# Performance work log

Hardware: AMD Instinct MI355X
Metric: run time of the kernel (lower is better)

The kernel has to match this reference:

```python
import math
import jax, jax.numpy as jnp
import numpy as np

NH = 16          # num_attention_heads
MAX_REL = 512    # max_relative_positions


def _t4(x):
    # [B, N, H] -> [B, NH, N, H/NH]  (transpose_for_scores)
    B, N, H = x.shape
    return x.reshape(B, N, NH, -1).transpose(0, 2, 1, 3)


def setup_inputs() -> dict:
    key = jax.random.key(0)
    ks = jax.random.split(key, 6)
    B, N, H = 1, 2048, 1024
    hidden_states = jax.random.normal(ks[0], (B, N, H), jnp.float32)
    attention_mask = jnp.ones((B, 1, N, N), jnp.int32)
    ids = jnp.arange(N, dtype=jnp.int32)
    relative_pos = ids[:, None] - ids[None, :]              # [N, N], build_relative_position
    rel_embeddings = jax.random.normal(ks[1], (2 * MAX_REL, H), jnp.float32) * 0.02
    in_proj_w = jax.random.normal(ks[2], (3 * H, H), jnp.float32) * 0.02
    q_bias = jnp.zeros((H,), jnp.float32)
    v_bias = jnp.zeros((H,), jnp.float32)
    pos_proj_w = jax.random.normal(ks[3], (H, H), jnp.float32) * 0.02
    pos_q_proj_w = jax.random.normal(ks[4], (H, H), jnp.float32) * 0.02
    pos_q_proj_b = jnp.zeros((H,), jnp.float32)
    return dict(hidden_states=hidden_states, attention_mask=attention_mask,
                relative_pos=relative_pos, rel_embeddings=rel_embeddings,
                in_proj_w=in_proj_w, q_bias=q_bias, v_bias=v_bias,
                pos_proj_w=pos_proj_w, pos_q_proj_w=pos_q_proj_w,
                pos_q_proj_b=pos_q_proj_b)


def reference(hidden_states, attention_mask, relative_pos, rel_embeddings,
              in_proj_w, q_bias, v_bias, pos_proj_w, pos_q_proj_w, pos_q_proj_b):
    B, N, H = hidden_states.shape
    dh = H // NH
    scale_factor = 1 + 2  # 1 + len(["c2p", "p2c"])
    scale = math.sqrt(dh * scale_factor)

    # fused QKV projection; chunk(3, dim=-1) AFTER transpose_for_scores -> per-head q|k|v layout
    qp = hidden_states @ in_proj_w.T                          # [B, N, 3H]
    q, k, v = jnp.split(_t4(qp), 3, axis=-1)                  # each [B, NH, N, dh]
    q = q + _t4(q_bias[None, None, :])
    v = v + _t4(v_bias[None, None, :])
    q = q / scale

    scores = jnp.einsum('bhqd,bhkd->bhqk', q, k)              # content-content

    # disentangled relative-position bias
    span = min(N, MAX_REL)                                    # att_span
    rel = rel_embeddings[MAX_REL - span:MAX_REL + span][None] # [1, 2S, H]
    rpos = relative_pos.astype(jnp.int32)[None, None]         # [1, 1, N, N]

    # c2p: content-to-position
    pos_k = _t4(rel @ pos_proj_w.T)                           # [1, NH, 2S, dh]
    c2p = jnp.einsum('bhqd,xhsd->bhqs', q, pos_k)             # [B, NH, N, 2S]
    c2p_pos = jnp.clip(rpos + span, 0, 2 * span - 1)
    c2p = jnp.take_along_axis(c2p, c2p_pos, axis=-1)          # gather -> [B, NH, N, N]

    # p2c: position-to-content
    pos_q = _t4(rel @ pos_q_proj_w.T + pos_q_proj_b) / scale  # [1, NH, 2S, dh]
    p2c = jnp.einsum('bhkd,xhsd->bhks', k, pos_q)             # [B, NH, N, 2S]
    p2c_pos = jnp.clip(-rpos + span, 0, 2 * span - 1)
    p2c = jnp.take_along_axis(p2c, p2c_pos, axis=-1)          # [B, NH, K, Q]
    p2c = jnp.swapaxes(p2c, -1, -2)                           # -> [B, NH, Q, K]

    scores = scores + c2p + p2c

    # XSoftmax: masked softmax, masked probs zeroed
    m = attention_mask.astype(bool)                           # [B, 1, N, N]
    probs = jax.nn.softmax(jnp.where(m, scores, -jnp.inf), axis=-1)
    probs = jnp.where(m, probs, 0.0)

    ctx = jnp.einsum('bhqk,bhkd->bhqd', probs, v)             # [B, NH, N, dh]
    return ctx.transpose(0, 2, 1, 3).reshape(B, N, H)
```

## Files before the change

kernel.cpp:

```cpp
#include <hip/hip_runtime.h>
#include <hip/hip_bf16.h>

typedef __bf16 bf16;
typedef __attribute__((ext_vector_type(8))) __bf16 bf16x8;
typedef __attribute__((ext_vector_type(8))) float f32x8;
typedef __attribute__((ext_vector_type(4))) float f32x4;

#define MFMA(a,b,c) __builtin_amdgcn_mfma_f32_16x16x32_bf16((a),(b),(c),0,0,0)

__device__ __forceinline__ bf16x8 ld8(const bf16* p){ bf16x8 v; __builtin_memcpy(&v,p,16); return v; }
__device__ __forceinline__ void   st8(bf16* p, bf16x8 v){ __builtin_memcpy(p,&v,16); }

__global__ __launch_bounds__(256)
void cvt_kernel(const float* __restrict__ s0, const float* __restrict__ s1,
                const float* __restrict__ s2, const float* __restrict__ s3,
                const float* __restrict__ s4,
                bf16* d0, bf16* d1, bf16* d2, bf16* d3, bf16* d4)
{
    const int sizes[5] = {2097152, 3145728, 1048576, 1048576, 1048576};
    const float* s; bf16* d;
    switch (blockIdx.y) {
        case 0: s = s0; d = d0; break;  case 1: s = s1; d = d1; break;
        case 2: s = s2; d = d2; break;  case 3: s = s3; d = d3; break;
        default: s = s4; d = d4;
    }
    const int n = sizes[blockIdx.y];
    const int stride = gridDim.x * 256 * 8;
    for (int i = (blockIdx.x * 256 + threadIdx.x) * 8; i < n; i += stride) {
        f32x8 v; __builtin_memcpy(&v, s + i, 32);
        bf16x8 r;
        #pragma unroll
        for (int j = 0; j < 8; j++) r[j] = (bf16)v[j];
        st8(d + i, r);
    }
}

__global__ __launch_bounds__(256)
void gemm_stage(const bf16* __restrict__ A, const bf16* __restrict__ Bpk,
                const bf16* __restrict__ Bpq, int K, int mode,
                const float* __restrict__ qb, const float* __restrict__ vb,
                bf16* __restrict__ o0, bf16* __restrict__ o1, bf16* __restrict__ o2,
                float* __restrict__ part)
{
    __shared__ __attribute__((aligned(16))) bf16 As[128][32];
    __shared__ __attribute__((aligned(16))) bf16 Bs[128][32];

    const int tid = threadIdx.x, w = tid >> 6, lane = tid & 63;
    const int l15 = lane & 15, quad = lane >> 4;
    const int wr = w >> 1, wc = w & 1;

    int arr = 0, my = blockIdx.y, kbeg = 0, kend = K;
    const bf16* B = Bpk;
    if (mode == 1) {
        arr = my >> 3; my &= 7;
        B = arr ? Bpq : Bpk;
        kbeg = blockIdx.z * 256; kend = kbeg + 256;
    }
    const int m0 = my * 128, n0 = blockIdx.x * 128;
    const int srow = tid >> 2, scol = (tid & 3) * 8;

    f32x4 acc[4][4] = {};
    for (int k0 = kbeg; k0 < kend; k0 += 32) {
        __syncthreads();
        st8(&As[srow][scol],    ld8(A + (size_t)(m0 + srow) * K + k0 + scol));
        st8(&As[srow+64][scol], ld8(A + (size_t)(m0 + 64 + srow) * K + k0 + scol));
        st8(&Bs[srow][scol],    ld8(B + (size_t)(n0 + srow) * K + k0 + scol));
        st8(&Bs[srow+64][scol], ld8(B + (size_t)(n0 + 64 + srow) * K + k0 + scol));
        __syncthreads();
        bf16x8 a[4], b[4];
        #pragma unroll
        for (int i = 0; i < 4; i++) a[i] = ld8(&As[wr*64 + i*16 + l15][quad*8]);
        #pragma unroll
        for (int j = 0; j < 4; j++) b[j] = ld8(&Bs[wc*64 + j*16 + l15][quad*8]);
        #pragma unroll
        for (int i = 0; i < 4; i++)
            #pragma unroll
            for (int j = 0; j < 4; j++)
                acc[i][j] = MFMA(a[i], b[j], acc[i][j]);
    }

    const float inv_scale = 0.07216878364870323f;
    #pragma unroll
    for (int i = 0; i < 4; i++) {
        #pragma unroll
        for (int j = 0; j < 4; j++) {
            #pragma unroll
            for (int r = 0; r < 4; r++) {
                int row = m0 + wr*64 + i*16 + quad*4 + r;
                int col = n0 + wc*64 + j*16 + l15;
                float v = acc[i][j][r];
                if (mode == 0) {
                    int h = col / 192, rr = col % 192;
                    if (rr < 64)
                        o0[((size_t)h*2048 + row)*64 + rr] =
                            (bf16)((v + qb[h*64 + rr]) * inv_scale);
                    else if (rr < 128)
                        o1[((size_t)h*2048 + row)*64 + (rr - 64)] = (bf16)v;
                    else
                        o2[((size_t)h*64 + (rr - 128))*2048 + row] =
                            (bf16)(v + vb[h*64 + (rr - 128)]);
                } else {
                    part[(((size_t)(arr*4 + blockIdx.z)*1024 + row)*1024) + col] = v;
                }
            }
        }
    }
}

__global__ __launch_bounds__(256)
void pos_merge(const float* __restrict__ part, const float* __restrict__ pqb,
               bf16* __restrict__ PKw, bf16* __restrict__ PQw)
{
    int e = blockIdx.x * 256 + threadIdx.x;
    int arr = e >> 20, r = (e >> 10) & 1023, c = e & 1023;
    const float* p = part + ((size_t)arr*4) * 1048576 + (size_t)r * 1024 + c;
    float v = p[0] + p[1048576] + p[2*1048576] + p[3*1048576];
    int h = c >> 6, d = c & 63;
    if (arr == 0) PKw[((size_t)h*1024 + r)*64 + d] = (bf16)v;
    else          PQw[((size_t)h*1024 + r)*64 + d] =
                      (bf16)((v + pqb[c]) * 0.07216878364870323f);
}

__global__ __launch_bounds__(256)
void edge_kernel(const bf16* __restrict__ Qw, const bf16* __restrict__ Kw,
                 const bf16* __restrict__ PKw, const bf16* __restrict__ PQw,
                 float* __restrict__ C2Pe, float* __restrict__ P2Ce)
{
    int t = blockIdx.x * 256 + threadIdx.x;
    int side = t >> 15, rest = t & 32767;
    int h = rest >> 11, n = rest & 2047;
    const bf16* row = (side ? Kw : Qw) + ((size_t)h*2048 + n) * 64;
    const bf16* eb  = (side ? PQw : PKw) + (size_t)h*1024*64;
    float a0 = 0.f, a1 = 0.f;
    #pragma unroll
    for (int c = 0; c < 8; c++) {
        bf16x8 x  = ld8(row + c*8);
        bf16x8 e0 = ld8(eb + c*8);
        bf16x8 e1 = ld8(eb + (size_t)1023*64 + c*8);
        #pragma unroll
        for (int j = 0; j < 8; j++) {
            a0 += (float)x[j] * (float)e0[j];
            a1 += (float)x[j] * (float)e1[j];
        }
    }
    float* o = side ? P2Ce : C2Pe;
    o[((size_t)h*2048 + n)*2 + 0] = a0;
    o[((size_t)h*2048 + n)*2 + 1] = a1;
}

#define KSPLIT 2

__global__ __launch_bounds__(64, 2)
void attn_kernel(const bf16* __restrict__ Q, const bf16* __restrict__ Kc,
                 const bf16* __restrict__ Vt, const bf16* __restrict__ PK,
                 const bf16* __restrict__ PQ,
                 const float* __restrict__ C2Pe, const float* __restrict__ P2Ce,
                 float* __restrict__ opart, float* __restrict__ pspart)
{
    __shared__ bf16 W1s[16][82];
    __shared__ bf16 W2s[2][16][82];
    __shared__ __attribute__((aligned(16))) bf16 Ps[16][72];

    const int lane = threadIdx.x;
    const int l15 = lane & 15, quad = lane >> 4;
    const int h = blockIdx.y, qw0 = blockIdx.x * 16, z = blockIdx.z;

    const bf16* Qh  = Q  + (size_t)h * 2048 * 64;
    const bf16* Kh  = Kc + (size_t)h * 2048 * 64;
    const bf16* Vh  = Vt + (size_t)h * 64 * 2048;
    const bf16* PKh = PK + (size_t)h * 1024 * 64;
    const bf16* PQh = PQ + (size_t)h * 1024 * 64;

    bf16x8 qa[2];
    #pragma unroll
    for (int s = 0; s < 2; s++)
        qa[s] = ld8(Qh + (size_t)(qw0 + l15)*64 + s*32 + quad*8);

    float c2pe0[4], c2pe1[4];
    #pragma unroll
    for (int r = 0; r < 4; r++) {
        int q = qw0 + quad*4 + r;
        c2pe0[r] = C2Pe[((size_t)h*2048 + q)*2 + 0];
        c2pe1[r] = C2Pe[((size_t)h*2048 + q)*2 + 1];
    }

    f32x4 oacc[4] = {};
    float psum[4] = {0.f, 0.f, 0.f, 0.f};

    for (int i = 0; i < 32 / KSPLIT; i++) {
        const int kb = z + i * KSPLIT;
        const int k0 = kb * 64;

        bf16x8 kf[4][2];
        #pragma unroll
        for (int nt = 0; nt < 4; nt++)
            #pragma unroll
            for (int s = 0; s < 2; s++)
                kf[nt][s] = ld8(Kh + (size_t)(k0 + nt*16 + l15)*64 + s*32 + quad*8);

        f32x4 sacc[4] = {};
        #pragma unroll
        for (int s = 0; s < 2; s++)
            #pragma unroll
            for (int nt = 0; nt < 4; nt++)
                sacc[nt] = MFMA(qa[s], kf[nt][s], sacc[nt]);

        float val[4][4];
        if (k0 >= qw0 + 527) {
            float p2[4];
            #pragma unroll
            for (int nt = 0; nt < 4; nt++)
                p2[nt] = P2Ce[((size_t)h*2048 + k0 + nt*16 + l15)*2 + 0];
            #pragma unroll
            for (int nt = 0; nt < 4; nt++)
                #pragma unroll
                for (int r = 0; r < 4; r++)
                    val[nt][r] = sacc[nt][r] + c2pe0[r] + p2[nt];
        } else if (k0 <= qw0 - 574) {
            float p2[4];
            #pragma unroll
            for (int nt = 0; nt < 4; nt++)
                p2[nt] = P2Ce[((size_t)h*2048 + k0 + nt*16 + l15)*2 + 1];
            #pragma unroll
            for (int nt = 0; nt < 4; nt++)
                #pragma unroll
                for (int r = 0; r < 4; r++)
                    val[nt][r] = sacc[nt][r] + c2pe1[r] + p2[nt];
        } else {
            const int winb = qw0 - k0 + 449;
            {
                f32x4 a1[5] = {};
                #pragma unroll
                for (int s = 0; s < 2; s++)
                    #pragma unroll
                    for (int n5 = 0; n5 < 5; n5++) {
                        int c = winb + n5*16 + l15;
                        c = min(max(c, 0), 1023);
                        bf16x8 bq = ld8(PKh + (size_t)c*64 + s*32 + quad*8);
                        a1[n5] = MFMA(qa[s], bq, a1[n5]);
                    }
                #pragma unroll
                for (int n5 = 0; n5 < 5; n5++)
                    #pragma unroll
                    for (int r = 0; r < 4; r++)
                        W1s[quad*4 + r][n5*16 + l15] = (bf16)a1[n5][r];
            }
            {
                bf16x8 pq[5][2];
                #pragma unroll
                for (int s = 0; s < 2; s++)
                    #pragma unroll
                    for (int n5 = 0; n5 < 5; n5++) {
                        int c = winb + n5*16 + l15;
                        c = min(max(c, 0), 1023);
                        pq[n5][s] = ld8(PQh + (size_t)c*64 + s*32 + quad*8);
                    }
                #pragma unroll
                for (int mt = 0; mt < 4; mt++) {
                    f32x4 a2[5] = {};
                    #pragma unroll
                    for (int s = 0; s < 2; s++)
                        #pragma unroll
                        for (int n5 = 0; n5 < 5; n5++)
                            a2[n5] = MFMA(kf[mt][s], pq[n5][s], a2[n5]);
                    #pragma unroll
                    for (int n5 = 0; n5 < 5; n5++)
                        #pragma unroll
                        for (int r = 0; r < 4; r++)
                            W2s[mt & 1][quad*4 + r][n5*16 + l15] = (bf16)a2[n5][r];
                    #pragma unroll
                    for (int r = 0; r < 4; r++) {
                        int off = quad*4 + r - mt*16 - l15 + 63;
                        val[mt][r] = sacc[mt][r] + (float)W1s[quad*4 + r][off]
                                                 + (float)W2s[mt & 1][l15][off];
                    }
                }
            }
        }

        #pragma unroll
        for (int nt = 0; nt < 4; nt++)
            #pragma unroll
            for (int r = 0; r < 4; r++) {
                float e = __expf(val[nt][r]);
                psum[r] += e;
                Ps[quad*4 + r][nt*16 + l15] = (bf16)e;
            }

        #pragma unroll
        for (int s = 0; s < 2; s++) {
            bf16x8 pa = ld8(&Ps[l15][s*32 + quad*8]);
            #pragma unroll
            for (int dt = 0; dt < 4; dt++) {
                bf16x8 vf = ld8(Vh + (size_t)(dt*16 + l15)*2048 + k0 + s*32 + quad*8);
                oacc[dt] = MFMA(pa, vf, oacc[dt]);
            }
        }
    }

    #pragma unroll
    for (int r = 0; r < 4; r++)
        #pragma unroll
        for (int m = 1; m < 16; m <<= 1)
            psum[r] += __shfl_xor(psum[r], m);

    const size_t zb = (size_t)(z * 16 + h);
    #pragma unroll
    for (int dt = 0; dt < 4; dt++)
        #pragma unroll
        for (int r = 0; r < 4; r++) {
            int row = qw0 + quad*4 + r;
            opart[(zb*2048 + row)*64 + dt*16 + l15] = oacc[dt][r];
        }
    if (l15 == 0) {
        #pragma unroll
        for (int r = 0; r < 4; r++)
            pspart[zb*2048 + qw0 + quad*4 + r] = psum[r];
    }
}

__global__ __launch_bounds__(256)
void attn_merge(const float* __restrict__ opart, const float* __restrict__ pspart,
                float* __restrict__ out)
{
    int t = blockIdx.x * 256 + threadIdx.x;
    int row = t >> 10, c = t & 1023, h = c >> 6, d = c & 63;
    float o = 0.f, p = 0.f;
    #pragma unroll
    for (int zz = 0; zz < KSPLIT; zz++) {
        size_t zb = (size_t)(zz * 16 + h);
        o += opart[(zb*2048 + row)*64 + d];
        p += pspart[zb*2048 + row];
    }
    out[t] = o / p;
}

extern "C" void kernel_launch(void* const* d_in, const int* in_sizes, int n_in,
                              void* d_out, int out_size, void* d_ws, size_t ws_size,
                              hipStream_t stream)
{
    (void)in_sizes; (void)n_in; (void)out_size; (void)ws_size;
    const float* X   = (const float*)d_in[0];
    const float* REL = (const float*)d_in[3];
    const float* Win = (const float*)d_in[4];
    const float* qb  = (const float*)d_in[5];
    const float* vb  = (const float*)d_in[6];
    const float* Wpk = (const float*)d_in[7];
    const float* Wpq = (const float*)d_in[8];
    const float* pqb = (const float*)d_in[9];
    float* out = (float*)d_out;

    char* ws = (char*)d_ws;
    const size_t MB = 1024u * 1024u;
    bf16*  Xb    = (bf16*)(ws);
    bf16*  Winb  = (bf16*)(ws + 4*MB);
    bf16*  Wpkb  = (bf16*)(ws + 10*MB);
    bf16*  Wpqb  = (bf16*)(ws + 12*MB);
    bf16*  RELb  = (bf16*)(ws + 14*MB);
    bf16*  Qw    = (bf16*)(ws + 16*MB);
    bf16*  Kw    = (bf16*)(ws + 20*MB);
    bf16*  Vtw   = (bf16*)(ws + 24*MB);
    bf16*  PKw   = (bf16*)(ws + 28*MB);
    bf16*  PQw   = (bf16*)(ws + 30*MB);
    float* Ppart = (float*)(ws + 32*MB);
    float* C2Pe  = (float*)(ws + 64*MB);
    float* P2Ce  = (float*)(ws + 64*MB + 256*1024);
    float* Opart  = (float*)(ws + 32*MB);
    float* PSpart = (float*)(ws + 14*MB);

    cvt_kernel<<<dim3(1536, 5), 256, 0, stream>>>(X, Win, Wpk, Wpq, REL,
                                                  Xb, Winb, Wpkb, Wpqb, RELb);
    gemm_stage<<<dim3(24, 16, 1), 256, 0, stream>>>(Xb, Winb, Winb, 1024, 0,
                                                    qb, vb, Qw, Kw, Vtw, nullptr);
    gemm_stage<<<dim3(8, 16, 4), 256, 0, stream>>>(RELb, Wpkb, Wpqb, 1024, 1,
                                                   nullptr, nullptr,
                                                   nullptr, nullptr, nullptr, Ppart);
    pos_merge<<<dim3(8192), 256, 0, stream>>>(Ppart, pqb, PKw, PQw);
    edge_kernel<<<dim3(256), 256, 0, stream>>>(Qw, Kw, PKw, PQw, C2Pe, P2Ce);
    attn_kernel<<<dim3(128, 16, KSPLIT), 64, 0, stream>>>(Qw, Kw, Vtw, PKw, PQw,
                                                          C2Pe, P2Ce, Opart, PSpart);
    attn_merge<<<dim3(8192), 256, 0, stream>>>(Opart, PSpart, out);
}
```

Baseline: 376.2 us.

## Precompute full p2c table per head and gather it inside attention

Adds a pos_tab kernel that computes K·PQ^T for every key and relative position per head (a 16×2048×1024 bf16 table). In the near-diagonal band, the attention kernel then gathers p2c values from this table instead of recomputing them with windowed MFMAs and an LDS staging buffer. The intent is to remove the redundant per-query-block p2c MFMA work and the W2s LDS round trip, and launch bounds are raised to allow more waves per SIMD. The cost is an extra 64MB table write and scattered global gathers in the band region, and the workspace layout is reshuffled to fit it.

```diff
diff --git a/kernel.cpp b/kernel.cpp
--- a/kernel.cpp
+++ b/kernel.cpp
@@ -122,6 +122,53 @@
 }
 
 __global__ __launch_bounds__(256)
+void pos_tab(const bf16* __restrict__ Kw, const bf16* __restrict__ PQw,
+             bf16* __restrict__ T)
+{
+    __shared__ __attribute__((aligned(16))) bf16 As[128][32];
+    __shared__ __attribute__((aligned(16))) bf16 Bs[128][32];
+
+    const int tid = threadIdx.x, w = tid >> 6, lane = tid & 63;
+    const int l15 = lane & 15, quad = lane >> 4;
+    const int wr = w >> 1, wc = w & 1;
+    const int h = blockIdx.z;
+    const int m0 = blockIdx.y * 128, n0 = blockIdx.x * 128;
+    const bf16* A = Kw  + (size_t)h * 2048 * 64;
+    const bf16* B = PQw + (size_t)h * 1024 * 64;
+    const int srow = tid >> 2, scol = (tid & 3) * 8;
+
+    f32x4 acc[4][4] = {};
+    for (int k0 = 0; k0 < 64; k0 += 32) {
+        __syncthreads();
+        st8(&As[srow][scol],    ld8(A + (size_t)(m0 + srow) * 64 + k0 + scol));
+        st8(&As[srow+64][scol], ld8(A + (size_t)(m0 + 64 + srow) * 64 + k0 + scol));
+        st8(&Bs[srow][scol],    ld8(B + (size_t)(n0 + srow) * 64 + k0 + scol));
+        st8(&Bs[srow+64][scol], ld8(B + (size_t)(n0 + 64 + srow) * 64 + k0 + scol));
+        __syncthreads();
+        bf16x8 a[4], b[4];
+        #pragma unroll
+        for (int i = 0; i < 4; i++) a[i] = ld8(&As[wr*64 + i*16 + l15][quad*8]);
+        #pragma unroll
+        for (int j = 0; j < 4; j++) b[j] = ld8(&Bs[wc*64 + j*16 + l15][quad*8]);
+        #pragma unroll
+        for (int i = 0; i < 4; i++)
+            #pragma unroll
+            for (int j = 0; j < 4; j++)
+                acc[i][j] = MFMA(a[i], b[j], acc[i][j]);
+    }
+
+    bf16* Th = T + (size_t)h * 2048 * 1024;
+    #pragma unroll
+    for (int i = 0; i < 4; i++)
+        #pragma unroll
+        for (int j = 0; j < 4; j++)
+            #pragma unroll
+            for (int r = 0; r < 4; r++)
+                Th[(size_t)(m0 + wr*64 + i*16 + quad*4 + r) * 1024
+                   + n0 + wc*64 + j*16 + l15] = (bf16)acc[i][j][r];
+}
+
+__global__ __launch_bounds__(256)
 void edge_kernel(const bf16* __restrict__ Qw, const bf16* __restrict__ Kw,
                  const bf16* __restrict__ PKw, const bf16* __restrict__ PQw,
                  float* __restrict__ C2Pe, float* __restrict__ P2Ce)
@@ -150,15 +197,14 @@
 
 #define KSPLIT 2
 
-__global__ __launch_bounds__(64, 2)
+__global__ __launch_bounds__(64, 4)
 void attn_kernel(const bf16* __restrict__ Q, const bf16* __restrict__ Kc,
                  const bf16* __restrict__ Vt, const bf16* __restrict__ PK,
-                 const bf16* __restrict__ PQ,
+                 const bf16* __restrict__ P2Ct,
                  const float* __restrict__ C2Pe, const float* __restrict__ P2Ce,
                  float* __restrict__ opart, float* __restrict__ pspart)
 {
     __shared__ bf16 W1s[16][82];
-    __shared__ bf16 W2s[2][16][82];
     __shared__ __attribute__((aligned(16))) bf16 Ps[16][72];
 
     const int lane = threadIdx.x;
@@ -169,20 +215,12 @@
     const bf16* Kh  = Kc + (size_t)h * 2048 * 64;
     const bf16* Vh  = Vt + (size_t)h * 64 * 2048;
     const bf16* PKh = PK + (size_t)h * 1024 * 64;
-    const bf16* PQh = PQ + (size_t)h * 1024 * 64;
+    const bf16* Pth = P2Ct + (size_t)h * 2048 * 1024;
 
     bf16x8 qa[2];
     #pragma unroll
     for (int s = 0; s < 2; s++)
         qa[s] = ld8(Qh + (size_t)(qw0 + l15)*64 + s*32 + quad*8);
-
-    float c2pe0[4], c2pe1[4];
-    #pragma unroll
-    for (int r = 0; r < 4; r++) {
-        int q = qw0 + quad*4 + r;
-        c2pe0[r] = C2Pe[((size_t)h*2048 + q)*2 + 0];
-        c2pe1[r] = C2Pe[((size_t)h*2048 + q)*2 + 1];
-    }
 
     f32x4 oacc[4] = {};
     float psum[4] = {0.f, 0.f, 0.f, 0.f};
@@ -205,27 +243,30 @@
             for (int nt = 0; nt < 4; nt++)
                 sacc[nt] = MFMA(qa[s], kf[nt][s], sacc[nt]);
 
-        float val[4][4];
         if (k0 >= qw0 + 527) {
-            float p2[4];
-            #pragma unroll
-            for (int nt = 0; nt < 4; nt++)
-                p2[nt] = P2Ce[((size_t)h*2048 + k0 + nt*16 + l15)*2 + 0];
-            #pragma unroll
-            for (int nt = 0; nt < 4; nt++)
+            float ce[4];
+            #pragma unroll
+            for (int r = 0; r < 4; r++)
+                ce[r] = C2Pe[((size_t)h*2048 + qw0 + quad*4 + r)*2 + 0];
+            #pragma unroll
+            for (int nt = 0; nt < 4; nt++) {
+                float p2 = P2Ce[((size_t)h*2048 + k0 + nt*16 + l15)*2 + 0];
                 #pragma unroll
                 for (int r = 0; r < 4; r++)
-                    val[nt][r] = sacc[nt][r] + c2pe0[r] + p2[nt];
+                    sacc[nt][r] += ce[r] + p2;
+            }
         } else if (k0 <= qw0 - 574) {
-            float p2[4];
-            #pragma unroll
-            for (int nt = 0; nt < 4; nt++)
-                p2[nt] = P2Ce[((size_t)h*2048 + k0 + nt*16 + l15)*2 + 1];
-            #pragma unroll
-            for (int nt = 0; nt < 4; nt++)
+            float ce[4];
+            #pragma unroll
+            for (int r = 0; r < 4; r++)
+                ce[r] = C2Pe[((size_t)h*2048 + qw0 + quad*4 + r)*2 + 1];
+            #pragma unroll
+            for (int nt = 0; nt < 4; nt++) {
+                float p2 = P2Ce[((size_t)h*2048 + k0 + nt*16 + l15)*2 + 1];
                 #pragma unroll
                 for (int r = 0; r < 4; r++)
-                    val[nt][r] = sacc[nt][r] + c2pe1[r] + p2[nt];
+                    sacc[nt][r] += ce[r] + p2;
+            }
         } else {
             const int winb = qw0 - k0 + 449;
             {
@@ -245,35 +286,15 @@
                     for (int r = 0; r < 4; r++)
                         W1s[quad*4 + r][n5*16 + l15] = (bf16)a1[n5][r];
             }
-            {
-                bf16x8 pq[5][2];
+            #pragma unroll
+            for (int nt = 0; nt < 4; nt++) {
+                const bf16* prow = Pth + (size_t)(k0 + nt*16 + l15) * 1024;
                 #pragma unroll
-                for (int s = 0; s < 2; s++)
-                    #pragma unroll
-                    for (int n5 = 0; n5 < 5; n5++) {
-                        int c = winb + n5*16 + l15;
-                        c = min(max(c, 0), 1023);
-                        pq[n5][s] = ld8(PQh + (size_t)c*64 + s*32 + quad*8);
-                    }
-                #pragma unroll
-                for (int mt = 0; mt < 4; mt++) {
-                    f32x4 a2[5] = {};
-                    #pragma unroll
-                    for (int s = 0; s < 2; s++)
-                        #pragma unroll
-                        for (int n5 = 0; n5 < 5; n5++)
-                            a2[n5] = MFMA(kf[mt][s], pq[n5][s], a2[n5]);
-                    #pragma unroll
-                    for (int n5 = 0; n5 < 5; n5++)
-                        #pragma unroll
-                        for (int r = 0; r < 4; r++)
-                            W2s[mt & 1][quad*4 + r][n5*16 + l15] = (bf16)a2[n5][r];
-                    #pragma unroll
-                    for (int r = 0; r < 4; r++) {
-                        int off = quad*4 + r - mt*16 - l15 + 63;
-                        val[mt][r] = sacc[mt][r] + (float)W1s[quad*4 + r][off]
-                                                 + (float)W2s[mt & 1][l15][off];
-                    }
+                for (int r = 0; r < 4; r++) {
+                    int off = quad*4 + r - nt*16 - l15 + 63;
+                    int idx = min(max(winb + off, 0), 1023);
+                    sacc[nt][r] += (float)W1s[quad*4 + r][off]
+                                 + (float)prow[idx];
                 }
             }
         }
@@ -282,7 +303,7 @@
         for (int nt = 0; nt < 4; nt++)
             #pragma unroll
             for (int r = 0; r < 4; r++) {
-                float e = __expf(val[nt][r]);
+                float e = __expf(sacc[nt][r]);
                 psum[r] += e;
                 Ps[quad*4 + r][nt*16 + l15] = (bf16)e;
             }
@@ -363,10 +384,11 @@
     bf16*  PKw   = (bf16*)(ws + 28*MB);
     bf16*  PQw   = (bf16*)(ws + 30*MB);
     float* Ppart = (float*)(ws + 32*MB);
-    float* C2Pe  = (float*)(ws + 64*MB);
-    float* P2Ce  = (float*)(ws + 64*MB + 256*1024);
-    float* Opart  = (float*)(ws + 32*MB);
-    float* PSpart = (float*)(ws + 14*MB);
+    bf16*  P2Ct  = (bf16*)(ws + 32*MB);
+    float* C2Pe  = (float*)(ws + 96*MB);
+    float* P2Ce  = (float*)(ws + 96*MB + 256*1024);
+    float* Opart  = (float*)(ws);
+    float* PSpart = (float*)(ws + 96*MB + 512*1024);
 
     cvt_kernel<<<dim3(1536, 5), 256, 0, stream>>>(X, Win, Wpk, Wpq, REL,
                                                   Xb, Winb, Wpkb, Wpqb, RELb);
@@ -376,8 +398,9 @@
                                                    nullptr, nullptr,
                                                    nullptr, nullptr, nullptr, Ppart);
     pos_merge<<<dim3(8192), 256, 0, stream>>>(Ppart, pqb, PKw, PQw);
+    pos_tab<<<dim3(8, 16, 16), 256, 0, stream>>>(Kw, PQw, P2Ct);
     edge_kernel<<<dim3(256), 256, 0, stream>>>(Qw, Kw, PKw, PQw, C2Pe, P2Ce);
-    attn_kernel<<<dim3(128, 16, KSPLIT), 64, 0, stream>>>(Qw, Kw, Vtw, PKw, PQw,
+    attn_kernel<<<dim3(128, 16, KSPLIT), 64, 0, stream>>>(Qw, Kw, Vtw, PKw, P2Ct,
                                                           C2Pe, P2Ce, Opart, PSpart);
     attn_merge<<<dim3(8192), 256, 0, stream>>>(Opart, PSpart, out);
 }
```

New measurement: 402.8 us. 7.1% more time.
